# Kernel optimization log

Measured on AMD Instinct MI355X. Metric: run time of the kernel, lower is better.

The kernel has to match this reference:

```python
import math
import jax, jax.numpy as jnp
import numpy as np

N_HEAD = 8
BLOCK_SIZE = 1024
LN_EPS = 1e-5


def _layer_norm(x, g, b):
    mu = jnp.mean(x, axis=-1, keepdims=True)
    var = jnp.var(x, axis=-1, keepdims=True)
    return (x - mu) * jax.lax.rsqrt(var + LN_EPS) * g + b


def _skew(QEr):
    # QEr: (B, nh, L, L) -> pad one zero column on the left, reshape, drop first row
    B, nh, nr, nc = QEr.shape
    padded = jnp.pad(QEr, ((0, 0), (0, 0), (0, 0), (1, 0)))  # (B, nh, nr, nc+1)
    reshaped = padded.reshape(B, nh, nc + 1, nr)
    return reshaped[:, :, 1:, :]  # (B, nh, nr, nc)


def _attn(x, W_qkv, b_qkv, W_o, b_o, Er):
    B, L, D = x.shape
    hs = D // N_HEAD
    qkv = x @ W_qkv + b_qkv  # (B, L, 3D)
    q, k, v = jnp.split(qkv, 3, axis=-1)
    # (B, nh, L, hs)
    q = q.reshape(B, L, N_HEAD, hs).transpose(0, 2, 1, 3)
    k = k.reshape(B, L, N_HEAD, hs).transpose(0, 2, 1, 3)
    v = v.reshape(B, L, N_HEAD, hs).transpose(0, 2, 1, 3)
    start = BLOCK_SIZE - L
    Er_t = Er[start:, :].T  # (hs, L)
    QEr = q @ Er_t  # (B, nh, L, L)
    Srel = _skew(QEr)
    scores = (jnp.einsum('bhqd,bhkd->bhqk', q, k) + Srel) * (1.0 / math.sqrt(hs))
    causal = jnp.tril(jnp.ones((L, L), dtype=bool))
    scores = jnp.where(causal, scores, jnp.float32(-jnp.inf))
    att = jax.nn.softmax(scores, axis=-1)
    y = jnp.einsum('bhqk,bhkd->bhqd', att, v)
    y = y.transpose(0, 2, 1, 3).reshape(B, L, D)
    return y @ W_o + b_o


def reference(x, W_qkv, b_qkv, W_o, b_o, Er, ln1_g, ln1_b, ln2_g, ln2_b,
              W_fc, b_fc, W_proj, b_proj):
    x = x + _attn(_layer_norm(x, ln1_g, ln1_b), W_qkv, b_qkv, W_o, b_o, Er)
    h = _layer_norm(x, ln2_g, ln2_b) @ W_fc + b_fc
    h = jax.nn.gelu(h, approximate=False)
    h = h @ W_proj + b_proj
    return x + h


def setup_inputs() -> dict:
    key = jax.random.key(0)
    ks = jax.random.split(key, 8)
    B, L, D, F = 8, 1024, 1024, 4096
    hs = D // N_HEAD
    s = lambda fan_in: 1.0 / math.sqrt(fan_in)
    return {
        'x': jax.random.normal(ks[0], (B, L, D), dtype=jnp.float32),
        'W_qkv': jax.random.normal(ks[1], (D, 3 * D), dtype=jnp.float32) * s(D),
        'b_qkv': jnp.zeros((3 * D,), dtype=jnp.float32),
        'W_o': jax.random.normal(ks[2], (D, D), dtype=jnp.float32) * s(D),
        'b_o': jnp.zeros((D,), dtype=jnp.float32),
        'Er': jax.random.normal(ks[3], (BLOCK_SIZE, hs), dtype=jnp.float32),
        'ln1_g': jnp.ones((D,), dtype=jnp.float32),
        'ln1_b': jnp.zeros((D,), dtype=jnp.float32),
        'ln2_g': jnp.ones((D,), dtype=jnp.float32),
        'ln2_b': jnp.zeros((D,), dtype=jnp.float32),
        'W_fc': jax.random.normal(ks[4], (D, F), dtype=jnp.float32) * s(D),
        'b_fc': jnp.zeros((F,), dtype=jnp.float32),
        'W_proj': jax.random.normal(ks[5], (F, D), dtype=jnp.float32) * s(F),
        'b_proj': jnp.zeros((D,), dtype=jnp.float32),
    }
```

## Files before the change

### kernel.cpp

```cpp
#include <hip/hip_runtime.h>
#include <hip/hip_bf16.h>
#include <math.h>

#define BB 8
#define LL 1024
#define DD 1024
#define FF 4096
#define NHH 8
#define HSS 128
#define SCALE 0.08838834764831845f
#define TRI(qi, kt) ((qi) * ((qi) + 1) / 2 + (kt))

typedef __bf16 bf16;
typedef __bf16 bf16x8 __attribute__((ext_vector_type(8)));
typedef float f32x4 __attribute__((ext_vector_type(4)));
typedef _Float16 f16;
typedef _Float16 f16x4 __attribute__((ext_vector_type(4)));

__device__ inline void async_copy16(const void* g, void* l) {
  __builtin_amdgcn_global_load_lds(
      (const __attribute__((address_space(1))) unsigned int*)g,
      (__attribute__((address_space(3))) unsigned int*)l, 16, 0, 0);
}

__global__ __launch_bounds__(256)
void transpose_cast_kernel(const float* __restrict__ W, bf16* __restrict__ Wt,
                           int K, int N) {
  __shared__ float tile[32][33];
  int n0 = blockIdx.x * 32, k0 = blockIdx.y * 32;
  int tx = threadIdx.x, ty = threadIdx.y;
#pragma unroll
  for (int i = 0; i < 32; i += 8)
    tile[ty + i][tx] = W[(size_t)(k0 + ty + i) * N + n0 + tx];
  __syncthreads();
#pragma unroll
  for (int i = 0; i < 32; i += 8)
    Wt[(size_t)(n0 + ty + i) * K + k0 + tx] = (bf16)tile[tx][ty + i];
}

__global__ __launch_bounds__(256)
void cast_bf16_kernel(const float* __restrict__ src, bf16* __restrict__ dst, int n) {
  int i = blockIdx.x * blockDim.x + threadIdx.x;
  if (i < n) dst[i] = (bf16)src[i];
}

__global__ __launch_bounds__(256)
void ln_kernel(const float* __restrict__ x, const float* __restrict__ g,
               const float* __restrict__ bta, bf16* __restrict__ out) {
  int row = blockIdx.x;
  int tid = threadIdx.x;
  const float4 v = ((const float4*)(x + (size_t)row * DD))[tid];
  float s = v.x + v.y + v.z + v.w;
  float s2 = v.x * v.x + v.y * v.y + v.z * v.z + v.w * v.w;
#pragma unroll
  for (int o = 32; o > 0; o >>= 1) {
    s += __shfl_down(s, o);
    s2 += __shfl_down(s2, o);
  }
  __shared__ float a1[4], a2[4];
  int wave = tid >> 6;
  if ((tid & 63) == 0) { a1[wave] = s; a2[wave] = s2; }
  __syncthreads();
  s = a1[0] + a1[1] + a1[2] + a1[3];
  s2 = a2[0] + a2[1] + a2[2] + a2[3];
  float mu = s * (1.0f / DD);
  float rstd = rsqrtf(s2 * (1.0f / DD) - mu * mu + 1e-5f);
  float4 gv = ((const float4*)g)[tid];
  float4 bv = ((const float4*)bta)[tid];
  bf16* o4 = out + (size_t)row * DD + tid * 4;
  o4[0] = (bf16)((v.x - mu) * rstd * gv.x + bv.x);
  o4[1] = (bf16)((v.y - mu) * rstd * gv.y + bv.y);
  o4[2] = (bf16)((v.z - mu) * rstd * gv.z + bv.z);
  o4[3] = (bf16)((v.w - mu) * rstd * gv.w + bv.w);
}

template <int EPI>
__global__ __launch_bounds__(256)
void gemm_kernel(const bf16* __restrict__ A, const bf16* __restrict__ Bt,
                 const float* __restrict__ bias, const float* __restrict__ res,
                 void* __restrict__ Cout, int M, int N, int K) {
  __shared__ bf16 Als[128 * 64];
  __shared__ bf16 Bls[128 * 64];
  int tid = threadIdx.x;
  int wave = tid >> 6, lane = tid & 63;
  int l15 = lane & 15, quad = lane >> 4;

  int m0 = blockIdx.y * 128, n0 = blockIdx.x * 128;
  int wm = (wave >> 1) * 64, wn = (wave & 1) * 64;
  f32x4 acc[4][4] = {};

  const bf16* asrc[4];
  const bf16* bsrc[4];
  int ldso[4];
#pragma unroll
  for (int i = 0; i < 4; i++) {
    int u = i * 256 + tid;
    int row = u >> 3, c = u & 7;
    int g = c ^ (row & 7);
    asrc[i] = A + (size_t)(m0 + row) * K + g * 8;
    bsrc[i] = Bt + (size_t)(n0 + row) * K + g * 8;
    ldso[i] = u * 8;
  }

  for (int k0 = 0; k0 < K; k0 += 64) {
    __syncthreads();
#pragma unroll
    for (int i = 0; i < 4; i++) {
      async_copy16(asrc[i] + k0, &Als[ldso[i]]);
      async_copy16(bsrc[i] + k0, &Bls[ldso[i]]);
    }
    __syncthreads();

    bf16x8 af[2][4], bfr[2][4];
#pragma unroll
    for (int kk = 0; kk < 2; kk++) {
#pragma unroll
      for (int mt = 0; mt < 4; mt++) {
        int ra = wm + mt * 16 + l15;
        af[kk][mt] = *(const bf16x8*)&Als[ra * 64 + (((kk * 4 + quad) ^ (ra & 7)) << 3)];
        int rb = wn + mt * 16 + l15;
        bfr[kk][mt] = *(const bf16x8*)&Bls[rb * 64 + (((kk * 4 + quad) ^ (rb & 7)) << 3)];
      }
    }
#pragma unroll
    for (int kk = 0; kk < 2; kk++)
#pragma unroll
      for (int mt = 0; mt < 4; mt++)
#pragma unroll
        for (int nt = 0; nt < 4; nt++)
          acc[mt][nt] = __builtin_amdgcn_mfma_f32_16x16x32_bf16(af[kk][mt], bfr[kk][nt],
                                                                acc[mt][nt], 0, 0, 0);
  }

#pragma unroll
  for (int mt = 0; mt < 4; mt++) {
#pragma unroll
    for (int nt = 0; nt < 4; nt++) {
      int col = n0 + wn + nt * 16 + l15;
      float bv = bias[col];
#pragma unroll
      for (int r = 0; r < 4; r++) {
        int row = m0 + wm + mt * 16 + quad * 4 + r;
        float v = acc[mt][nt][r] + bv;
        if (EPI == 1) v = 0.5f * v * (1.0f + erff(v * 0.7071067811865475f));
        if (EPI == 2) {
          v += res[(size_t)row * N + col];
          ((float*)Cout)[(size_t)row * N + col] = v;
        } else {
          ((bf16*)Cout)[(size_t)row * N + col] = (bf16)v;
        }
      }
    }
  }
}

__global__ __launch_bounds__(256)
void pack_kv_kernel(const bf16* __restrict__ qkv, bf16* __restrict__ Kpack,
                    bf16* __restrict__ Vpack) {
  __shared__ bf16 Vst[64][132];
  int kt = blockIdx.x, h = blockIdx.y, b = blockIdx.z;
  int tid = threadIdx.x;
  const size_t rs = 3 * DD;
  const bf16* kb = qkv + (size_t)b * LL * rs + (size_t)(kt * 64) * rs + DD + h * HSS;
  const bf16* vb = kb + DD;
  bf16* kp = Kpack + ((size_t)(b * NHH + h) * 16 + kt) * (64 * 128);
  bf16* vp = Vpack + ((size_t)(b * NHH + h) * 16 + kt) * (128 * 64);
#pragma unroll
  for (int i = 0; i < 4; i++) {
    int u = i * 256 + tid;
    int kk = u >> 4, c = u & 15;
    bf16x8 kv = *(const bf16x8*)(kb + (size_t)kk * rs + c * 8);
    *(bf16x8*)(kp + kk * 128 + ((c ^ kk) & 15) * 8) = kv;
    *(bf16x8*)&Vst[kk][c * 8] = *(const bf16x8*)(vb + (size_t)kk * rs + c * 8);
  }
  __syncthreads();
#pragma unroll
  for (int i = 0; i < 4; i++) {
    int u = i * 256 + tid;
    int d = u >> 3, c = u & 7;
    bf16x8 t;
#pragma unroll
    for (int j = 0; j < 8; j++) t[j] = Vst[c * 8 + j][d];
    *(bf16x8*)(vp + d * 64 + ((c ^ (d & 7))) * 8) = t;
  }
}

__global__ __launch_bounds__(256)
void relband_kernel(const bf16* __restrict__ qkv, const bf16* __restrict__ Erb,
                    f16* __restrict__ band) {
  int t = blockIdx.x;
  int h = blockIdx.y, b = blockIdx.z;
  int qi = (int)((sqrtf((float)(8 * t + 1)) - 1.0f) * 0.5f);
  while (TRI(qi + 1, 0) <= t) qi++;
  while (TRI(qi, 0) > t) qi--;
  int kt = t - TRI(qi, 0);

  int tid = threadIdx.x, wave = tid >> 6, lane = tid & 63;
  int l15 = lane & 15, quad = lane >> 4;
  int qw0 = qi * 64 + wave * 16;
  int k0 = kt * 64;
  const size_t rs = 3 * DD;
  const bf16* qbase = qkv + (size_t)b * LL * rs + h * HSS;
  bf16x8 qf[4];
#pragma unroll
  for (int st = 0; st < 4; st++)
    qf[st] = *(const bf16x8*)(qbase + (size_t)(qw0 + l15) * rs + st * 32 + quad * 8);

  int kmax_off = qw0 + 15 - k0;
  int m_base = 1008 - qw0 + k0;
  int ntR = (kmax_off >> 4) + 1;
  if (ntR > 4) ntR = 4;
  f32x4 rr[5] = {};
#pragma unroll
  for (int n = 0; n < 5; n++) {
    if (n <= ntR) {
      int mr = m_base + n * 16 + l15;
      mr = mr < 0 ? 0 : (mr > 1023 ? 1023 : mr);
#pragma unroll
      for (int st = 0; st < 4; st++) {
        bf16x8 ef = *(const bf16x8*)(Erb + (size_t)mr * HSS + st * 32 + quad * 8);
        rr[n] = __builtin_amdgcn_mfma_f32_16x16x32_bf16(qf[st], ef, rr[n], 0, 0, 0);
      }
    }
  }
  f16x4 sf[4];
#pragma unroll
  for (int rg = 0; rg < 4; rg++) {
    int qloc = quad * 4 + rg;
    int tt = 15 - qloc + l15;
    int src = (lane & 48) | (tt & 15);
    float shv[5];
#pragma unroll
    for (int n = 0; n < 5; n++)
      shv[n] = (n <= ntR) ? __shfl(rr[n][rg], src) : 0.f;
#pragma unroll
    for (int nt = 0; nt < 4; nt++)
      sf[nt][rg] = (f16)((tt & 16) ? shv[nt + 1] : shv[nt]);
  }
  f16* tb = band + (size_t)(b * NHH + h) * (136 * 4096) + (size_t)t * 4096;
#pragma unroll
  for (int nt = 0; nt < 4; nt++)
    if (nt * 16 <= kmax_off)
      *(f16x4*)(tb + (wave * 4 + nt) * 256 + l15 * 16 + quad * 4) = sf[nt];
}

__global__ __launch_bounds__(256)
void flash_kernel(const bf16* __restrict__ qkv, const bf16* __restrict__ Kpack,
                  const bf16* __restrict__ Vpack, const f16* __restrict__ band,
                  bf16* __restrict__ y) {
  __shared__ bf16 Kls[2][64 * 128];
  __shared__ bf16 Vls[2][128 * 64];
  __shared__ bf16 Pls[4][16][72];

  int tid = threadIdx.x, wave = tid >> 6, lane = tid & 63;
  int l15 = lane & 15, quad = lane >> 4;
  int h = blockIdx.y, b = blockIdx.z;

  const size_t rs = 3 * DD;
  const bf16* qbase = qkv + (size_t)b * LL * rs + h * HSS;
  const bf16* kp = Kpack + (size_t)(b * NHH + h) * 16 * (64 * 128);
  const bf16* vp = Vpack + (size_t)(b * NHH + h) * 16 * (128 * 64);
  const f16* bnd = band + (size_t)(b * NHH + h) * (136 * 4096);

  int buf = 0;
#pragma unroll 1
  for (int ph = 0; ph < 2; ph++) {
    int qb = ph ? 15 - blockIdx.x : blockIdx.x;
    int qw0 = qb * 64 + wave * 16;
    int nkt = qb + 1;

    bf16x8 qf[4];
#pragma unroll
    for (int st = 0; st < 4; st++)
      qf[st] = *(const bf16x8*)(qbase + (size_t)(qw0 + l15) * rs + st * 32 + quad * 8);

    {
      const bf16* ks = kp;
      const bf16* vs = vp;
#pragma unroll
      for (int i = 0; i < 4; i++) {
        int off = (wave * 4 + i) * 512 + lane * 8;
        async_copy16(ks + off, &Kls[buf][off]);
        async_copy16(vs + off, &Vls[buf][off]);
      }
    }

    f32x4 o[8] = {};
    float mrow[4] = {-INFINITY, -INFINITY, -INFINITY, -INFINITY};
    float lrow[4] = {0.f, 0.f, 0.f, 0.f};

#pragma unroll 1
    for (int kt = 0; kt < nkt; kt++) {
      int k0 = kt * 64;
      int kmax_off = qw0 + 15 - k0;
      __syncthreads();

      const f16* tb = bnd + (size_t)TRI(qb, kt) * 4096;
      f16x4 srl[4] = {};
#pragma unroll
      for (int nt = 0; nt < 4; nt++)
        if (nt * 16 <= kmax_off)
          srl[nt] = *(const f16x4*)(tb + (wave * 4 + nt) * 256 + l15 * 16 + quad * 4);

      if (kt + 1 < nkt) {
        const bf16* ks = kp + (size_t)(kt + 1) * (64 * 128);
        const bf16* vs = vp + (size_t)(kt + 1) * (128 * 64);
#pragma unroll
        for (int i = 0; i < 4; i++) {
          int off = (wave * 4 + i) * 512 + lane * 8;
          async_copy16(ks + off, &Kls[buf ^ 1][off]);
          async_copy16(vs + off, &Vls[buf ^ 1][off]);
        }
      }

      f32x4 sa[4] = {};
#pragma unroll
      for (int nt = 0; nt < 4; nt++) {
        if (nt * 16 <= kmax_off) {
          int kk = nt * 16 + l15;
#pragma unroll
          for (int st = 0; st < 4; st++) {
            bf16x8 kf = *(const bf16x8*)&Kls[buf][kk * 128 + (((st * 4 + quad) ^ l15) & 15) * 8];
            sa[nt] = __builtin_amdgcn_mfma_f32_16x16x32_bf16(qf[st], kf, sa[nt], 0, 0, 0);
          }
        }
      }

      float pmx[4] = {-INFINITY, -INFINITY, -INFINITY, -INFINITY};
#pragma unroll
      for (int nt = 0; nt < 4; nt++) {
        if (nt * 16 <= kmax_off) {
          int kg = k0 + nt * 16 + l15;
#pragma unroll
          for (int rg = 0; rg < 4; rg++) {
            int qg = qw0 + quad * 4 + rg;
            float v = (sa[nt][rg] + (float)srl[nt][rg]) * SCALE;
            v = (kg <= qg) ? v : -INFINITY;
            sa[nt][rg] = v;
            pmx[rg] = fmaxf(pmx[rg], v);
          }
        } else {
#pragma unroll
          for (int rg = 0; rg < 4; rg++) sa[nt][rg] = -INFINITY;
        }
      }

#pragma unroll
      for (int rg = 0; rg < 4; rg++) {
        float v = pmx[rg];
        v = fmaxf(v, __shfl_xor(v, 1));
        v = fmaxf(v, __shfl_xor(v, 2));
        v = fmaxf(v, __shfl_xor(v, 4));
        v = fmaxf(v, __shfl_xor(v, 8));
        float mnew = fmaxf(mrow[rg], v);
        float alpha = __expf(mrow[rg] - mnew);
        mrow[rg] = mnew;
        lrow[rg] *= alpha;
#pragma unroll
        for (int nt = 0; nt < 8; nt++) o[nt][rg] *= alpha;
        pmx[rg] = mnew;
      }
      float ls[4] = {0.f, 0.f, 0.f, 0.f};
#pragma unroll
      for (int nt = 0; nt < 4; nt++)
#pragma unroll
        for (int rg = 0; rg < 4; rg++) {
          float p = __expf(sa[nt][rg] - pmx[rg]);
          ls[rg] += p;
          Pls[wave][quad * 4 + rg][nt * 16 + l15] = (bf16)p;
        }
#pragma unroll
      for (int rg = 0; rg < 4; rg++) {
        float v = ls[rg];
        v += __shfl_xor(v, 1);
        v += __shfl_xor(v, 2);
        v += __shfl_xor(v, 4);
        v += __shfl_xor(v, 8);
        lrow[rg] += v;
      }

      bf16x8 pf[2];
#pragma unroll
      for (int s2 = 0; s2 < 2; s2++)
        pf[s2] = *(const bf16x8*)&Pls[wave][l15][s2 * 32 + quad * 8];
#pragma unroll
      for (int nt = 0; nt < 8; nt++) {
        int d = nt * 16 + l15;
#pragma unroll
        for (int s2 = 0; s2 < 2; s2++) {
          if (s2 * 32 <= kmax_off) {
            bf16x8 vf = *(const bf16x8*)&Vls[buf][d * 64 + (((s2 * 4 + quad) ^ (l15 & 7)) & 7) * 8];
            o[nt] = __builtin_amdgcn_mfma_f32_16x16x32_bf16(pf[s2], vf, o[nt], 0, 0, 0);
          }
        }
      }
      buf ^= 1;
    }

#pragma unroll
    for (int rg = 0; rg < 4; rg++) {
      float inv = 1.0f / lrow[rg];
      int qg = qw0 + quad * 4 + rg;
      bf16* yr = y + ((size_t)b * LL + qg) * DD + h * HSS;
#pragma unroll
      for (int nt = 0; nt < 8; nt++) yr[nt * 16 + l15] = (bf16)(o[nt][rg] * inv);
    }
  }
}

extern "C" void kernel_launch(void* const* d_in, const int* in_sizes, int n_in,
                              void* d_out, int out_size, void* d_ws, size_t ws_size,
                              hipStream_t stream) {
  const float* x = (const float*)d_in[0];
  const float* W_qkv = (const float*)d_in[1];
  const float* b_qkv = (const float*)d_in[2];
  const float* W_o = (const float*)d_in[3];
  const float* b_o = (const float*)d_in[4];
  const float* Er = (const float*)d_in[5];
  const float* ln1_g = (const float*)d_in[6];
  const float* ln1_b = (const float*)d_in[7];
  const float* ln2_g = (const float*)d_in[8];
  const float* ln2_b = (const float*)d_in[9];
  const float* W_fc = (const float*)d_in[10];
  const float* b_fc = (const float*)d_in[11];
  const float* W_proj = (const float*)d_in[12];
  const float* b_proj = (const float*)d_in[13];
  float* out = (float*)d_out;

  char* p = (char*)d_ws;
  auto alloc = [&](size_t bytes) {
    char* r = p;
    p += (bytes + 255) & ~(size_t)255;
    return r;
  };
  bf16* Wt_qkv = (bf16*)alloc((size_t)3072 * 1024 * 2);
  bf16* Wt_o   = (bf16*)alloc((size_t)1024 * 1024 * 2);
  bf16* Wt_fc  = (bf16*)alloc((size_t)4096 * 1024 * 2);
  bf16* Wt_pr  = (bf16*)alloc((size_t)1024 * 4096 * 2);
  bf16* Erb    = (bf16*)alloc((size_t)1024 * 128 * 2);
  bf16* xn     = (bf16*)alloc((size_t)8192 * 1024 * 2);
  bf16* qkvb   = (bf16*)alloc((size_t)8192 * 3072 * 2);
  bf16* yb     = (bf16*)alloc((size_t)8192 * 1024 * 2);
  bf16* Kpack  = (bf16*)alloc((size_t)64 * 16 * 64 * 128 * 2);
  bf16* Vpack  = (bf16*)alloc((size_t)64 * 16 * 128 * 64 * 2);
  f16*  band   = (f16*)alloc((size_t)64 * 136 * 4096 * 2);
  float* x2    = (float*)band;
  bf16* hb     = qkvb;

  transpose_cast_kernel<<<dim3(3072 / 32, 1024 / 32), dim3(32, 8), 0, stream>>>(W_qkv, Wt_qkv, 1024, 3072);
  transpose_cast_kernel<<<dim3(1024 / 32, 1024 / 32), dim3(32, 8), 0, stream>>>(W_o, Wt_o, 1024, 1024);
  transpose_cast_kernel<<<dim3(4096 / 32, 1024 / 32), dim3(32, 8), 0, stream>>>(W_fc, Wt_fc, 1024, 4096);
  transpose_cast_kernel<<<dim3(1024 / 32, 4096 / 32), dim3(32, 8), 0, stream>>>(W_proj, Wt_pr, 4096, 1024);
  cast_bf16_kernel<<<512, 256, 0, stream>>>(Er, Erb, 1024 * 128);

  ln_kernel<<<8192, 256, 0, stream>>>(x, ln1_g, ln1_b, xn);
  gemm_kernel<0><<<dim3(24, 64), 256, 0, stream>>>(xn, Wt_qkv, b_qkv, nullptr, qkvb, 8192, 3072, 1024);
  pack_kv_kernel<<<dim3(16, 8, 8), 256, 0, stream>>>(qkvb, Kpack, Vpack);
  relband_kernel<<<dim3(136, 8, 8), 256, 0, stream>>>(qkvb, Erb, band);
  flash_kernel<<<dim3(8, 8, 8), 256, 0, stream>>>(qkvb, Kpack, Vpack, band, yb);
  gemm_kernel<2><<<dim3(8, 64), 256, 0, stream>>>(yb, Wt_o, b_o, x, x2, 8192, 1024, 1024);
  ln_kernel<<<8192, 256, 0, stream>>>(x2, ln2_g, ln2_b, xn);
  gemm_kernel<1><<<dim3(32, 64), 256, 0, stream>>>(xn, Wt_fc, b_fc, nullptr, hb, 8192, 4096, 1024);
  gemm_kernel<2><<<dim3(8, 64), 256, 0, stream>>>(hb, Wt_pr, b_proj, x2, out, 8192, 1024, 4096);
}
```

Baseline: 659.7 us.

## Fuse relative-position band computation into flash attention kernel

Removes the separate relband kernel, which wrote a precomputed fp16 skewed Q·Er band to global memory. The flash kernel now loads Er rows directly, computes the Q·Er MFMA tile and applies the skew shuffle inline per key tile. This saves a launch and roughly 71MB of band write and read traffic. In exchange the flash kernel does extra MFMA work and Er loads inside its loop, raising register pressure (ef[5][4] held live) and possibly lowering occupancy. x2 now gets its own allocation instead of aliasing the band buffer.

```diff
diff --git a/kernel.cpp b/kernel.cpp
--- a/kernel.cpp
+++ b/kernel.cpp
@@ -186,67 +186,8 @@
 }
 
 __global__ __launch_bounds__(256)
-void relband_kernel(const bf16* __restrict__ qkv, const bf16* __restrict__ Erb,
-                    f16* __restrict__ band) {
-  int t = blockIdx.x;
-  int h = blockIdx.y, b = blockIdx.z;
-  int qi = (int)((sqrtf((float)(8 * t + 1)) - 1.0f) * 0.5f);
-  while (TRI(qi + 1, 0) <= t) qi++;
-  while (TRI(qi, 0) > t) qi--;
-  int kt = t - TRI(qi, 0);
-
-  int tid = threadIdx.x, wave = tid >> 6, lane = tid & 63;
-  int l15 = lane & 15, quad = lane >> 4;
-  int qw0 = qi * 64 + wave * 16;
-  int k0 = kt * 64;
-  const size_t rs = 3 * DD;
-  const bf16* qbase = qkv + (size_t)b * LL * rs + h * HSS;
-  bf16x8 qf[4];
-#pragma unroll
-  for (int st = 0; st < 4; st++)
-    qf[st] = *(const bf16x8*)(qbase + (size_t)(qw0 + l15) * rs + st * 32 + quad * 8);
-
-  int kmax_off = qw0 + 15 - k0;
-  int m_base = 1008 - qw0 + k0;
-  int ntR = (kmax_off >> 4) + 1;
-  if (ntR > 4) ntR = 4;
-  f32x4 rr[5] = {};
-#pragma unroll
-  for (int n = 0; n < 5; n++) {
-    if (n <= ntR) {
-      int mr = m_base + n * 16 + l15;
-      mr = mr < 0 ? 0 : (mr > 1023 ? 1023 : mr);
-#pragma unroll
-      for (int st = 0; st < 4; st++) {
-        bf16x8 ef = *(const bf16x8*)(Erb + (size_t)mr * HSS + st * 32 + quad * 8);
-        rr[n] = __builtin_amdgcn_mfma_f32_16x16x32_bf16(qf[st], ef, rr[n], 0, 0, 0);
-      }
-    }
-  }
-  f16x4 sf[4];
-#pragma unroll
-  for (int rg = 0; rg < 4; rg++) {
-    int qloc = quad * 4 + rg;
-    int tt = 15 - qloc + l15;
-    int src = (lane & 48) | (tt & 15);
-    float shv[5];
-#pragma unroll
-    for (int n = 0; n < 5; n++)
-      shv[n] = (n <= ntR) ? __shfl(rr[n][rg], src) : 0.f;
-#pragma unroll
-    for (int nt = 0; nt < 4; nt++)
-      sf[nt][rg] = (f16)((tt & 16) ? shv[nt + 1] : shv[nt]);
-  }
-  f16* tb = band + (size_t)(b * NHH + h) * (136 * 4096) + (size_t)t * 4096;
-#pragma unroll
-  for (int nt = 0; nt < 4; nt++)
-    if (nt * 16 <= kmax_off)
-      *(f16x4*)(tb + (wave * 4 + nt) * 256 + l15 * 16 + quad * 4) = sf[nt];
-}
-
-__global__ __launch_bounds__(256)
 void flash_kernel(const bf16* __restrict__ qkv, const bf16* __restrict__ Kpack,
-                  const bf16* __restrict__ Vpack, const f16* __restrict__ band,
+                  const bf16* __restrict__ Vpack, const bf16* __restrict__ Erb,
                   bf16* __restrict__ y) {
   __shared__ bf16 Kls[2][64 * 128];
   __shared__ bf16 Vls[2][128 * 64];
@@ -260,7 +201,6 @@
   const bf16* qbase = qkv + (size_t)b * LL * rs + h * HSS;
   const bf16* kp = Kpack + (size_t)(b * NHH + h) * 16 * (64 * 128);
   const bf16* vp = Vpack + (size_t)(b * NHH + h) * 16 * (128 * 64);
-  const f16* bnd = band + (size_t)(b * NHH + h) * (136 * 4096);
 
   int buf = 0;
 #pragma unroll 1
@@ -293,14 +233,22 @@
     for (int kt = 0; kt < nkt; kt++) {
       int k0 = kt * 64;
       int kmax_off = qw0 + 15 - k0;
+      int m_base = 1008 - qw0 + k0;
+      int ntR = (kmax_off >> 4) + 1;
+      if (ntR > 4) ntR = 4;
       __syncthreads();
 
-      const f16* tb = bnd + (size_t)TRI(qb, kt) * 4096;
-      f16x4 srl[4] = {};
-#pragma unroll
-      for (int nt = 0; nt < 4; nt++)
-        if (nt * 16 <= kmax_off)
-          srl[nt] = *(const f16x4*)(tb + (wave * 4 + nt) * 256 + l15 * 16 + quad * 4);
+      bf16x8 ef[5][4];
+#pragma unroll
+      for (int n = 0; n < 5; n++) {
+        if (n <= ntR) {
+          int mr = m_base + n * 16 + l15;
+          mr = mr < 0 ? 0 : (mr > 1023 ? 1023 : mr);
+#pragma unroll
+          for (int st = 0; st < 4; st++)
+            ef[n][st] = *(const bf16x8*)(Erb + (size_t)mr * HSS + st * 32 + quad * 8);
+        }
+      }
 
       if (kt + 1 < nkt) {
         const bf16* ks = kp + (size_t)(kt + 1) * (64 * 128);
@@ -313,6 +261,16 @@
         }
       }
 
+      f32x4 rr[5] = {};
+#pragma unroll
+      for (int n = 0; n < 5; n++) {
+        if (n <= ntR) {
+#pragma unroll
+          for (int st = 0; st < 4; st++)
+            rr[n] = __builtin_amdgcn_mfma_f32_16x16x32_bf16(qf[st], ef[n][st], rr[n], 0, 0, 0);
+        }
+      }
+
       f32x4 sa[4] = {};
 #pragma unroll
       for (int nt = 0; nt < 4; nt++) {
@@ -328,20 +286,27 @@
 
       float pmx[4] = {-INFINITY, -INFINITY, -INFINITY, -INFINITY};
 #pragma unroll
-      for (int nt = 0; nt < 4; nt++) {
-        if (nt * 16 <= kmax_off) {
-          int kg = k0 + nt * 16 + l15;
-#pragma unroll
-          for (int rg = 0; rg < 4; rg++) {
-            int qg = qw0 + quad * 4 + rg;
-            float v = (sa[nt][rg] + (float)srl[nt][rg]) * SCALE;
+      for (int rg = 0; rg < 4; rg++) {
+        int qloc = quad * 4 + rg;
+        int qg = qw0 + qloc;
+        int tt = 15 - qloc + l15;
+        int src = (lane & 48) | (tt & 15);
+        float shv[5];
+#pragma unroll
+        for (int n = 0; n < 5; n++)
+          shv[n] = (n <= ntR) ? __shfl(rr[n][rg], src) : 0.f;
+#pragma unroll
+        for (int nt = 0; nt < 4; nt++) {
+          if (nt * 16 <= kmax_off) {
+            int kg = k0 + nt * 16 + l15;
+            float srel = (tt & 16) ? shv[nt + 1] : shv[nt];
+            float v = (sa[nt][rg] + srel) * SCALE;
             v = (kg <= qg) ? v : -INFINITY;
             sa[nt][rg] = v;
             pmx[rg] = fmaxf(pmx[rg], v);
+          } else {
+            sa[nt][rg] = -INFINITY;
           }
-        } else {
-#pragma unroll
-          for (int rg = 0; rg < 4; rg++) sa[nt][rg] = -INFINITY;
         }
       }
 
@@ -443,8 +408,7 @@
   bf16* yb     = (bf16*)alloc((size_t)8192 * 1024 * 2);
   bf16* Kpack  = (bf16*)alloc((size_t)64 * 16 * 64 * 128 * 2);
   bf16* Vpack  = (bf16*)alloc((size_t)64 * 16 * 128 * 64 * 2);
-  f16*  band   = (f16*)alloc((size_t)64 * 136 * 4096 * 2);
-  float* x2    = (float*)band;
+  float* x2    = (float*)alloc((size_t)8192 * 1024 * 4);
   bf16* hb     = qkvb;
 
   transpose_cast_kernel<<<dim3(3072 / 32, 1024 / 32), dim3(32, 8), 0, stream>>>(W_qkv, Wt_qkv, 1024, 3072);
@@ -456,8 +420,7 @@
   ln_kernel<<<8192, 256, 0, stream>>>(x, ln1_g, ln1_b, xn);
   gemm_kernel<0><<<dim3(24, 64), 256, 0, stream>>>(xn, Wt_qkv, b_qkv, nullptr, qkvb, 8192, 3072, 1024);
   pack_kv_kernel<<<dim3(16, 8, 8), 256, 0, stream>>>(qkvb, Kpack, Vpack);
-  relband_kernel<<<dim3(136, 8, 8), 256, 0, stream>>>(qkvb, Erb, band);
-  flash_kernel<<<dim3(8, 8, 8), 256, 0, stream>>>(qkvb, Kpack, Vpack, band, yb);
+  flash_kernel<<<dim3(8, 8, 8), 256, 0, stream>>>(qkvb, Kpack, Vpack, Erb, yb);
   gemm_kernel<2><<<dim3(8, 64), 256, 0, stream>>>(yb, Wt_o, b_o, x, x2, 8192, 1024, 1024);
   ln_kernel<<<8192, 256, 0, stream>>>(x2, ln2_g, ln2_b, xn);
   gemm_kernel<1><<<dim3(32, 64), 256, 0, stream>>>(xn, Wt_fc, b_fc, nullptr, hb, 8192, 4096, 1024);
```

Result: slower. 715.8 us (+8.5%).

## Pack Er in MFMA fragment order and loop relband tiles per persistent block

Applied to the files above, without the earlier changes.

Er is converted to bf16 in a layout that matches the MFMA B-fragment order, in groups of 16 rows, so each lane loads a contiguous 16 bytes per step. The relband kernel no longer launches one block per triangular tile (136 per head). It now launches 8 blocks per head, and each block handles a pair of query blocks (qb and 15-qb) so the work is balanced. Each block loads its Q fragment once per query block and loops over the key tiles. This removes the sqrt-based index decode and repeated Q loads. The cost is fewer blocks (512 in total), which may reduce occupancy and latency hiding for this kernel. The clamping also changes from row granularity to group granularity.

```diff
diff --git a/kernel.cpp b/kernel.cpp
--- a/kernel.cpp
+++ b/kernel.cpp
@@ -39,9 +39,13 @@
 }
 
 __global__ __launch_bounds__(256)
-void cast_bf16_kernel(const float* __restrict__ src, bf16* __restrict__ dst, int n) {
-  int i = blockIdx.x * blockDim.x + threadIdx.x;
-  if (i < n) dst[i] = (bf16)src[i];
+void pack_er_kernel(const float* __restrict__ Er, bf16* __restrict__ ErP) {
+  int g = blockIdx.x, tid = threadIdx.x;
+  int l15 = tid & 15, quad = (tid >> 4) & 3, st = tid >> 6;
+  const float* src = Er + (size_t)(g * 16 + l15) * HSS + st * 32 + quad * 8;
+  bf16* dst = ErP + (size_t)g * 2048 + tid * 8;
+#pragma unroll
+  for (int j = 0; j < 8; j++) dst[j] = (bf16)src[j];
 }
 
 __global__ __launch_bounds__(256)
@@ -186,62 +190,70 @@
 }
 
 __global__ __launch_bounds__(256)
-void relband_kernel(const bf16* __restrict__ qkv, const bf16* __restrict__ Erb,
+void relband_kernel(const bf16* __restrict__ qkv, const bf16* __restrict__ ErP,
                     f16* __restrict__ band) {
-  int t = blockIdx.x;
-  int h = blockIdx.y, b = blockIdx.z;
-  int qi = (int)((sqrtf((float)(8 * t + 1)) - 1.0f) * 0.5f);
-  while (TRI(qi + 1, 0) <= t) qi++;
-  while (TRI(qi, 0) > t) qi--;
-  int kt = t - TRI(qi, 0);
-
   int tid = threadIdx.x, wave = tid >> 6, lane = tid & 63;
   int l15 = lane & 15, quad = lane >> 4;
-  int qw0 = qi * 64 + wave * 16;
-  int k0 = kt * 64;
+  int h = blockIdx.y, b = blockIdx.z;
   const size_t rs = 3 * DD;
   const bf16* qbase = qkv + (size_t)b * LL * rs + h * HSS;
-  bf16x8 qf[4];
-#pragma unroll
-  for (int st = 0; st < 4; st++)
-    qf[st] = *(const bf16x8*)(qbase + (size_t)(qw0 + l15) * rs + st * 32 + quad * 8);
-
-  int kmax_off = qw0 + 15 - k0;
-  int m_base = 1008 - qw0 + k0;
-  int ntR = (kmax_off >> 4) + 1;
-  if (ntR > 4) ntR = 4;
-  f32x4 rr[5] = {};
-#pragma unroll
-  for (int n = 0; n < 5; n++) {
-    if (n <= ntR) {
-      int mr = m_base + n * 16 + l15;
-      mr = mr < 0 ? 0 : (mr > 1023 ? 1023 : mr);
-#pragma unroll
-      for (int st = 0; st < 4; st++) {
-        bf16x8 ef = *(const bf16x8*)(Erb + (size_t)mr * HSS + st * 32 + quad * 8);
-        rr[n] = __builtin_amdgcn_mfma_f32_16x16x32_bf16(qf[st], ef, rr[n], 0, 0, 0);
-      }
-    }
-  }
-  f16x4 sf[4];
-#pragma unroll
-  for (int rg = 0; rg < 4; rg++) {
-    int qloc = quad * 4 + rg;
-    int tt = 15 - qloc + l15;
-    int src = (lane & 48) | (tt & 15);
-    float shv[5];
-#pragma unroll
-    for (int n = 0; n < 5; n++)
-      shv[n] = (n <= ntR) ? __shfl(rr[n][rg], src) : 0.f;
-#pragma unroll
-    for (int nt = 0; nt < 4; nt++)
-      sf[nt][rg] = (f16)((tt & 16) ? shv[nt + 1] : shv[nt]);
-  }
-  f16* tb = band + (size_t)(b * NHH + h) * (136 * 4096) + (size_t)t * 4096;
-#pragma unroll
-  for (int nt = 0; nt < 4; nt++)
-    if (nt * 16 <= kmax_off)
-      *(f16x4*)(tb + (wave * 4 + nt) * 256 + l15 * 16 + quad * 4) = sf[nt];
+  f16* bbase = band + (size_t)(b * NHH + h) * (136 * 4096);
+
+#pragma unroll 1
+  for (int ph = 0; ph < 2; ph++) {
+    int qb = ph ? 15 - blockIdx.x : blockIdx.x;
+    int qw0 = qb * 64 + wave * 16;
+
+    bf16x8 qf[4];
+#pragma unroll
+    for (int st = 0; st < 4; st++)
+      qf[st] = *(const bf16x8*)(qbase + (size_t)(qw0 + l15) * rs + st * 32 + quad * 8);
+
+#pragma unroll 1
+    for (int kt = 0; kt <= qb; kt++) {
+      int k0 = kt * 64;
+      int kmax_off = qw0 + 15 - k0;
+      int m_base = 1008 - qw0 + k0;
+      int gb = m_base >> 4;
+      int ntR = (kmax_off >> 4) + 1;
+      if (ntR > 4) ntR = 4;
+
+      f32x4 rr[5] = {};
+#pragma unroll
+      for (int n = 0; n < 5; n++) {
+        if (n <= ntR) {
+          int g = gb + n;
+          if (g > 63) g = 63;
+          const bf16* ep = ErP + (size_t)g * 2048 + lane * 8;
+#pragma unroll
+          for (int st = 0; st < 4; st++) {
+            bf16x8 ef = *(const bf16x8*)(ep + st * 512);
+            rr[n] = __builtin_amdgcn_mfma_f32_16x16x32_bf16(qf[st], ef, rr[n], 0, 0, 0);
+          }
+        }
+      }
+
+      f16x4 sf[4];
+#pragma unroll
+      for (int rg = 0; rg < 4; rg++) {
+        int qloc = quad * 4 + rg;
+        int tt = 15 - qloc + l15;
+        int src = (lane & 48) | (tt & 15);
+        float shv[5];
+#pragma unroll
+        for (int n = 0; n < 5; n++)
+          shv[n] = (n <= ntR) ? __shfl(rr[n][rg], src) : 0.f;
+#pragma unroll
+        for (int nt = 0; nt < 4; nt++)
+          sf[nt][rg] = (f16)((tt & 16) ? shv[nt + 1] : shv[nt]);
+      }
+      f16* tb = bbase + (size_t)TRI(qb, kt) * 4096;
+#pragma unroll
+      for (int nt = 0; nt < 4; nt++)
+        if (nt * 16 <= kmax_off)
+          *(f16x4*)(tb + (wave * 4 + nt) * 256 + l15 * 16 + quad * 4) = sf[nt];
+    }
+  }
 }
 
 __global__ __launch_bounds__(256)
@@ -437,7 +449,7 @@
   bf16* Wt_o   = (bf16*)alloc((size_t)1024 * 1024 * 2);
   bf16* Wt_fc  = (bf16*)alloc((size_t)4096 * 1024 * 2);
   bf16* Wt_pr  = (bf16*)alloc((size_t)1024 * 4096 * 2);
-  bf16* Erb    = (bf16*)alloc((size_t)1024 * 128 * 2);
+  bf16* ErP    = (bf16*)alloc((size_t)1024 * 128 * 2);
   bf16* xn     = (bf16*)alloc((size_t)8192 * 1024 * 2);
   bf16* qkvb   = (bf16*)alloc((size_t)8192 * 3072 * 2);
   bf16* yb     = (bf16*)alloc((size_t)8192 * 1024 * 2);
@@ -451,12 +463,12 @@
   transpose_cast_kernel<<<dim3(1024 / 32, 1024 / 32), dim3(32, 8), 0, stream>>>(W_o, Wt_o, 1024, 1024);
   transpose_cast_kernel<<<dim3(4096 / 32, 1024 / 32), dim3(32, 8), 0, stream>>>(W_fc, Wt_fc, 1024, 4096);
   transpose_cast_kernel<<<dim3(1024 / 32, 4096 / 32), dim3(32, 8), 0, stream>>>(W_proj, Wt_pr, 4096, 1024);
-  cast_bf16_kernel<<<512, 256, 0, stream>>>(Er, Erb, 1024 * 128);
+  pack_er_kernel<<<64, 256, 0, stream>>>(Er, ErP);
 
   ln_kernel<<<8192, 256, 0, stream>>>(x, ln1_g, ln1_b, xn);
   gemm_kernel<0><<<dim3(24, 64), 256, 0, stream>>>(xn, Wt_qkv, b_qkv, nullptr, qkvb, 8192, 3072, 1024);
   pack_kv_kernel<<<dim3(16, 8, 8), 256, 0, stream>>>(qkvb, Kpack, Vpack);
-  relband_kernel<<<dim3(136, 8, 8), 256, 0, stream>>>(qkvb, Erb, band);
+  relband_kernel<<<dim3(8, 8, 8), 256, 0, stream>>>(qkvb, ErP, band);
   flash_kernel<<<dim3(8, 8, 8), 256, 0, stream>>>(qkvb, Kpack, Vpack, band, yb);
   gemm_kernel<2><<<dim3(8, 64), 256, 0, stream>>>(yb, Wt_o, b_o, x, x2, 8192, 1024, 1024);
   ln_kernel<<<8192, 256, 0, stream>>>(x2, ln2_g, ln2_b, xn);
```

Result: faster. 616.5 us (-6.5%).
